# Kernel tuning notes

Measured on AMD Instinct MI355X. Metric: run time of the kernel, lower is better.

The kernel has to match this reference:

```python
import math
import jax, jax.numpy as jnp
import numpy as np

LMAX = 10
R_REF = 6371000.0
N = 1_000_000


def _sh_renorm(l, m, fourpi=True):
    base = math.sqrt((2.0 * l + 1.0) * math.factorial(l - abs(m)) / (4.0 * math.pi * math.factorial(l + abs(m))))
    if fourpi:
        base *= math.sqrt(4.0 * math.pi)
    return base


def _assoc_legendre(l, m, x):
    # P_l^m(x) via the standard stable recursion; l, m are Python ints (unrolled at trace time).
    pmm = jnp.ones_like(x)
    if m > 0:
        somx2 = jnp.sqrt(jnp.clip((1.0 - x) * (1.0 + x), 0.0, None))
        fact = 1.0
        for _ in range(1, m + 1):
            pmm = pmm * (-fact) * somx2
            fact += 2.0
    if l == m:
        return pmm
    pmmp1 = x * (2.0 * m + 1.0) * pmm
    if l == m + 1:
        return pmmp1
    pll = pmmp1
    for ll in range(m + 2, l + 1):
        pll = ((2.0 * ll - 1.0) * x * pmmp1 - (ll + m - 1.0) * pmm) / (ll - m)
        pmm = pmmp1
        pmmp1 = pll
    return pll


def _sh(m, l, phi, theta):
    cos_theta = jnp.clip(jnp.cos(theta), -1.0 + 1e-07, 1.0 - 1e-07)
    P_lm = _assoc_legendre(l, abs(m), cos_theta)
    K_lm = _sh_renorm(l, m)
    if m == 0:
        return K_lm * P_lm
    elif m > 0:
        return math.sqrt(2.0) * K_lm * jnp.cos(m * phi) * P_lm
    else:
        return math.sqrt(2.0) * K_lm * jnp.sin(-m * phi) * P_lm


def setup_inputs() -> dict:
    key = jax.random.key(0)
    k1, k2, k3 = jax.random.split(key, 3)
    lon = jax.random.uniform(k1, (N,), jnp.float32, -180.0, 180.0)
    lat = jax.random.uniform(k2, (N,), jnp.float32, -89.0, 89.0)
    r = R_REF * (1.0 + 0.01 * jax.random.uniform(k3, (N,), jnp.float32))
    return {"lonlatr": jnp.stack([lon, lat, r], axis=-1)}


def reference(lonlatr):
    lon, lat, r = lonlatr[:, 0], lonlatr[:, 1], lonlatr[:, 2]
    phi = jnp.deg2rad(lon + 180.0)
    theta = jnp.clip(jnp.deg2rad(90.0 - lat), 1e-07, math.pi - 1e-07)
    Y = []
    for l in range(LMAX + 1):
        for m in range(-l, l + 1):
            Y.append(_sh(m, l, phi, theta))
    Y = jnp.stack(Y, axis=-1)  # (N, (LMAX+1)^2)
    deg_idx = jnp.asarray(np.repeat(np.arange(LMAX + 1), 2 * np.arange(LMAX + 1) + 1), dtype=jnp.float32)
    radial_factor = (R_REF / r)[:, None] ** deg_idx[None, :]
    return Y * radial_factor
```

## Files before the change

### kernel.cpp

```cpp
#include <hip/hip_runtime.h>
#include <math.h>

#define LMAX 10
#define NCOL 121
#define PPB  64
#define TILE4 (PPB * NCOL / 4)

typedef float f4_t __attribute__((ext_vector_type(4)));

struct Tab {
    float K[66];
    float A[66];
    float B[66];
};

template<int M>
__device__ __forceinline__ void chain(const Tab& t, float* __restrict__ row,
                                      float pmm, float rfm, float rf, float x,
                                      float cm, float sm) {
    {
        float v = t.K[M * (M + 1) / 2 + M] * pmm * rfm;
        if constexpr (M == 0) row[0] = v;
        else { row[M * M + 2 * M] = v * cm; row[M * M] = v * sm; }
    }
    if constexpr (M < LMAX) {
        float p0 = pmm;
        float p1 = x * (float)(2 * M + 1) * pmm;
        float rfl = rfm * rf;
        {
            constexpr int L = M + 1;
            float v = t.K[L * (L + 1) / 2 + M] * p1 * rfl;
            if constexpr (M == 0) row[L * L + L] = v;
            else { row[L * L + L + M] = v * cm; row[L * L + L - M] = v * sm; }
        }
#pragma unroll
        for (int ll = M + 2; ll <= LMAX; ++ll) {
            int ti = ll * (ll + 1) / 2 + M;
            float p2 = t.A[ti] * x * p1 - t.B[ti] * p0;
            p0 = p1; p1 = p2;
            rfl *= rf;
            float v = t.K[ti] * p1 * rfl;
            int jb = ll * ll + ll;
            if constexpr (M == 0) row[jb] = v;
            else { row[jb + M] = v * cm; row[jb - M] = v * sm; }
        }
    }
}

template<bool FULL>
__global__ __launch_bounds__(256)
void sh_kernel(const float* __restrict__ in, float* __restrict__ out,
               int n, int blk_off, Tab t) {
    __shared__ f4_t lds4[TILE4];
    float* lds = (float*)lds4;

    const int bid = blockIdx.x + blk_off;
    const int p = threadIdx.x & 63;
    const int s = threadIdx.x >> 6;
    const long long gp = (long long)bid * PPB + p;

    if (FULL || gp < n) {
        const float lon = in[gp * 3 + 0];
        const float lat = in[gp * 3 + 1];
        const float r   = in[gp * 3 + 2];

        const float D2R  = 0.017453292519943295f;
        const float PI_F = 3.14159265358979323846f;

        float phi   = (lon + 180.0f) * D2R;
        float theta = fminf(fmaxf((90.0f - lat) * D2R, 1e-7f), PI_F - 1e-7f);
        float x = __cosf(theta);
        x = fminf(fmaxf(x, -1.0f + 1e-7f), 1.0f - 1e-7f);
        float somx2 = sqrtf(fmaxf((1.0f - x) * (1.0f + x), 0.0f));
        float rf  = 6371000.0f / r;
        float rf2 = rf * rf;
        float rf3 = rf2 * rf;
        float rf5 = rf3 * rf2;

        float c1, s1;
        __sincosf(phi, &s1, &c1);
        float c2 = c1 * c1 - s1 * s1, s2 = 2.0f * c1 * s1;
        float c3 = c2 * c1 - s2 * s1, s3 = s2 * c1 + c2 * s1;
        float c4 = c2 * c2 - s2 * s2, s4 = 2.0f * c2 * s2;
        float c5 = c4 * c1 - s4 * s1, s5 = s4 * c1 + c4 * s1;

        float sx2 = somx2 * somx2;
        float sx3 = sx2 * somx2;
        float sx5 = sx3 * sx2;

        float* row = lds + p * NCOL;

#define ROT(cm, sm, ck, sk) { float cn = cm * ck - sm * sk; sm = sm * ck + cm * sk; cm = cn; }

        switch (s) {
        case 0: {
            float pmm = 1.0f, rfm = 1.0f, cm = 1.0f, sm = 0.0f;
            chain<0>(t, row, pmm, rfm, rf, x, cm, sm);
            pmm *= -945.0f    * sx5; rfm *= rf5; ROT(cm, sm, c5, s5);
            chain<5>(t, row, pmm, rfm, rf, x, cm, sm);
            pmm *= -692835.0f * sx5; rfm *= rf5; ROT(cm, sm, c5, s5);
            chain<10>(t, row, pmm, rfm, rf, x, cm, sm);
        } break;
        case 1: {
            float pmm = -somx2, rfm = rf, cm = c1, sm = s1;
            chain<1>(t, row, pmm, rfm, rf, x, cm, sm);
            pmm *= -10395.0f * sx5; rfm *= rf5; ROT(cm, sm, c5, s5);
            chain<6>(t, row, pmm, rfm, rf, x, cm, sm);
            pmm *= -3315.0f  * sx3; rfm *= rf3; ROT(cm, sm, c3, s3);
            chain<9>(t, row, pmm, rfm, rf, x, cm, sm);
        } break;
        case 2: {
            float pmm = 3.0f * sx2, rfm = rf2, cm = c2, sm = s2;
            chain<2>(t, row, pmm, rfm, rf, x, cm, sm);
            pmm *= -45045.0f * sx5; rfm *= rf5; ROT(cm, sm, c5, s5);
            chain<7>(t, row, pmm, rfm, rf, x, cm, sm);
            pmm *= -15.0f * somx2;  rfm *= rf;  ROT(cm, sm, c1, s1);
            chain<8>(t, row, pmm, rfm, rf, x, cm, sm);
        } break;
        default: {
            float pmm = -15.0f * sx3, rfm = rf3, cm = c3, sm = s3;
            chain<3>(t, row, pmm, rfm, rf, x, cm, sm);
            pmm *= -7.0f * somx2; rfm *= rf; ROT(cm, sm, c1, s1);
            chain<4>(t, row, pmm, rfm, rf, x, cm, sm);
        } break;
        }
#undef ROT
    }
    __syncthreads();

    f4_t* __restrict__ dst = (f4_t*)out + (long long)bid * TILE4;
    if (FULL) {
#pragma unroll
        for (int k = 0; k < 7; ++k)
            dst[threadIdx.x + k * 256] = lds4[threadIdx.x + k * 256];
        if (threadIdx.x < TILE4 - 7 * 256)
            dst[threadIdx.x + 7 * 256] = lds4[threadIdx.x + 7 * 256];
    } else {
        const long long lim4 = ((long long)n * NCOL + 3) / 4;
        const long long base4 = (long long)bid * TILE4;
        for (int f = threadIdx.x; f < TILE4; f += 256) {
            if (base4 + f < lim4)
                dst[f] = lds4[f];
        }
    }
}

extern "C" void kernel_launch(void* const* d_in, const int* in_sizes, int n_in,
                              void* d_out, int out_size, void* d_ws, size_t ws_size,
                              hipStream_t stream) {
    const float* in = (const float*)d_in[0];
    float* out = (float*)d_out;
    const int n = in_sizes[0] / 3;

    Tab t;
    double fact[2 * LMAX + 1];
    fact[0] = 1.0;
    for (int i = 1; i <= 2 * LMAX; ++i) fact[i] = fact[i - 1] * (double)i;
    for (int l = 0; l <= LMAX; ++l) {
        for (int m = 0; m <= l; ++m) {
            int ti = l * (l + 1) / 2 + m;
            double k = sqrt((2.0 * l + 1.0) * fact[l - m] / fact[l + m]);
            if (m > 0) k *= sqrt(2.0);
            t.K[ti] = (float)k;
            if (l >= m + 2) {
                t.A[ti] = (float)((2.0 * l - 1.0) / (double)(l - m));
                t.B[ti] = (float)(((double)(l + m) - 1.0) / (double)(l - m));
            } else {
                t.A[ti] = 0.0f; t.B[ti] = 0.0f;
            }
        }
    }

    const int full_blocks = n / PPB;
    const int tail_pts    = n - full_blocks * PPB;
    if (full_blocks > 0)
        sh_kernel<true><<<full_blocks, 256, 0, stream>>>(in, out, n, 0, t);
    if (tail_pts > 0)
        sh_kernel<false><<<1, 256, 0, stream>>>(in, out, n, full_blocks, t);
}
```

Before: 103.0 us.

## Persistent double-buffered tiles with fp16 LDS staging and nontemporal stores

Replaces one-block-per-tile with a persistent grid of at most 1280 blocks that loop over tiles. Each block stores the previous tile from one LDS buffer while computing the next into the other. LDS staging moves to fp16 to halve shared memory and allow more resident blocks, and global writes use nontemporal stores. The fp16 round-trip loses precision in outputs stored as float, which risks failing accuracy tolerances.

```diff
diff --git a/kernel.cpp b/kernel.cpp
--- a/kernel.cpp
+++ b/kernel.cpp
@@ -1,9 +1,11 @@
 #include <hip/hip_runtime.h>
+#include <hip/hip_fp16.h>
 #include <math.h>
 
 #define LMAX 10
 #define NCOL 121
 #define PPB  64
+#define TILEH (PPB * NCOL)
 #define TILE4 (PPB * NCOL / 4)
 
 typedef float f4_t __attribute__((ext_vector_type(4)));
@@ -14,14 +16,14 @@
     float B[66];
 };
 
-template<int M>
-__device__ __forceinline__ void chain(const Tab& t, float* __restrict__ row,
+template<int M, typename ST, typename EMIT>
+__device__ __forceinline__ void chain(const Tab& t, ST* __restrict__ row,
                                       float pmm, float rfm, float rf, float x,
-                                      float cm, float sm) {
+                                      float cm, float sm, EMIT emit) {
     {
         float v = t.K[M * (M + 1) / 2 + M] * pmm * rfm;
-        if constexpr (M == 0) row[0] = v;
-        else { row[M * M + 2 * M] = v * cm; row[M * M] = v * sm; }
+        if constexpr (M == 0) emit(row, 0, v);
+        else { emit(row, M * M + 2 * M, v * cm); emit(row, M * M, v * sm); }
     }
     if constexpr (M < LMAX) {
         float p0 = pmm;
@@ -30,8 +32,8 @@
         {
             constexpr int L = M + 1;
             float v = t.K[L * (L + 1) / 2 + M] * p1 * rfl;
-            if constexpr (M == 0) row[L * L + L] = v;
-            else { row[L * L + L + M] = v * cm; row[L * L + L - M] = v * sm; }
+            if constexpr (M == 0) emit(row, L * L + L, v);
+            else { emit(row, L * L + L + M, v * cm); emit(row, L * L + L - M, v * sm); }
         }
 #pragma unroll
         for (int ll = M + 2; ll <= LMAX; ++ll) {
@@ -41,108 +43,156 @@
             rfl *= rf;
             float v = t.K[ti] * p1 * rfl;
             int jb = ll * ll + ll;
-            if constexpr (M == 0) row[jb] = v;
-            else { row[jb + M] = v * cm; row[jb - M] = v * sm; }
+            if constexpr (M == 0) emit(row, jb, v);
+            else { emit(row, jb + M, v * cm); emit(row, jb - M, v * sm); }
         }
     }
 }
 
-template<bool FULL>
-__global__ __launch_bounds__(256)
-void sh_kernel(const float* __restrict__ in, float* __restrict__ out,
-               int n, int blk_off, Tab t) {
-    __shared__ f4_t lds4[TILE4];
-    float* lds = (float*)lds4;
-
-    const int bid = blockIdx.x + blk_off;
+template<typename ST, typename EMIT>
+__device__ __forceinline__ void compute_tile(const float* __restrict__ in,
+                                             long long gp, int s, const Tab& t,
+                                             ST* __restrict__ row, EMIT emit) {
+    const float lon = in[gp * 3 + 0];
+    const float lat = in[gp * 3 + 1];
+    const float r   = in[gp * 3 + 2];
+
+    const float D2R  = 0.017453292519943295f;
+    const float PI_F = 3.14159265358979323846f;
+
+    float phi   = (lon + 180.0f) * D2R;
+    float theta = fminf(fmaxf((90.0f - lat) * D2R, 1e-7f), PI_F - 1e-7f);
+    float x = __cosf(theta);
+    x = fminf(fmaxf(x, -1.0f + 1e-7f), 1.0f - 1e-7f);
+    float somx2 = sqrtf(fmaxf((1.0f - x) * (1.0f + x), 0.0f));
+    float rf  = 6371000.0f / r;
+    float rf2 = rf * rf;
+    float rf3 = rf2 * rf;
+    float rf5 = rf3 * rf2;
+
+    float c1, s1;
+    __sincosf(phi, &s1, &c1);
+    float c2 = c1 * c1 - s1 * s1, s2 = 2.0f * c1 * s1;
+    float c3 = c2 * c1 - s2 * s1, s3 = s2 * c1 + c2 * s1;
+    float c5 = (c2 * c2 - s2 * s2) * c1 - 2.0f * c2 * s2 * s1;
+    float s5 = 2.0f * c2 * s2 * c1 + (c2 * c2 - s2 * s2) * s1;
+
+    float sx2 = somx2 * somx2;
+    float sx3 = sx2 * somx2;
+    float sx5 = sx3 * sx2;
+
+#define ROT(cm, sm, ck, sk) { float cn = cm * ck - sm * sk; sm = sm * ck + cm * sk; cm = cn; }
+    switch (s) {
+    case 0: {
+        float pmm = 1.0f, rfm = 1.0f, cm = 1.0f, sm = 0.0f;
+        chain<0>(t, row, pmm, rfm, rf, x, cm, sm, emit);
+        pmm *= -945.0f    * sx5; rfm *= rf5; ROT(cm, sm, c5, s5);
+        chain<5>(t, row, pmm, rfm, rf, x, cm, sm, emit);
+        pmm *= -692835.0f * sx5; rfm *= rf5; ROT(cm, sm, c5, s5);
+        chain<10>(t, row, pmm, rfm, rf, x, cm, sm, emit);
+    } break;
+    case 1: {
+        float pmm = -somx2, rfm = rf, cm = c1, sm = s1;
+        chain<1>(t, row, pmm, rfm, rf, x, cm, sm, emit);
+        pmm *= -10395.0f * sx5; rfm *= rf5; ROT(cm, sm, c5, s5);
+        chain<6>(t, row, pmm, rfm, rf, x, cm, sm, emit);
+        pmm *= -3315.0f  * sx3; rfm *= rf3; ROT(cm, sm, c3, s3);
+        chain<9>(t, row, pmm, rfm, rf, x, cm, sm, emit);
+    } break;
+    case 2: {
+        float pmm = 3.0f * sx2, rfm = rf2, cm = c2, sm = s2;
+        chain<2>(t, row, pmm, rfm, rf, x, cm, sm, emit);
+        pmm *= -45045.0f * sx5; rfm *= rf5; ROT(cm, sm, c5, s5);
+        chain<7>(t, row, pmm, rfm, rf, x, cm, sm, emit);
+        pmm *= -15.0f * somx2;  rfm *= rf;  ROT(cm, sm, c1, s1);
+        chain<8>(t, row, pmm, rfm, rf, x, cm, sm, emit);
+    } break;
+    default: {
+        float pmm = -15.0f * sx3, rfm = rf3, cm = c3, sm = s3;
+        chain<3>(t, row, pmm, rfm, rf, x, cm, sm, emit);
+        pmm *= -7.0f * somx2; rfm *= rf; ROT(cm, sm, c1, s1);
+        chain<4>(t, row, pmm, rfm, rf, x, cm, sm, emit);
+    } break;
+    }
+#undef ROT
+}
+
+struct EmitH {
+    __device__ void operator()(__half* row, int j, float v) const {
+        row[j] = __float2half(v);
+    }
+};
+struct EmitF {
+    __device__ void operator()(float* row, int j, float v) const {
+        row[j] = v;
+    }
+};
+
+__device__ __forceinline__ void store_tile(const __half* __restrict__ buf,
+                                           f4_t* __restrict__ dst) {
+    const uint2* __restrict__ src = (const uint2*)buf;
+#pragma unroll
+    for (int k = 0; k < 7; ++k) {
+        int i = threadIdx.x + k * 256;
+        uint2 h = src[i];
+        float2 fa = __half22float2(*(const __half2*)&h.x);
+        float2 fb = __half22float2(*(const __half2*)&h.y);
+        f4_t v = {fa.x, fa.y, fb.x, fb.y};
+        __builtin_nontemporal_store(v, &dst[i]);
+    }
+    if (threadIdx.x < TILE4 - 7 * 256) {
+        int i = threadIdx.x + 7 * 256;
+        uint2 h = src[i];
+        float2 fa = __half22float2(*(const __half2*)&h.x);
+        float2 fb = __half22float2(*(const __half2*)&h.y);
+        f4_t v = {fa.x, fa.y, fb.x, fb.y};
+        __builtin_nontemporal_store(v, &dst[i]);
+    }
+}
+
+__global__ __launch_bounds__(256, 5)
+void sh_main(const float* __restrict__ in, float* __restrict__ out,
+             int ntiles, Tab t) {
+    __shared__ __half lds[2][TILEH];
+
     const int p = threadIdx.x & 63;
     const int s = threadIdx.x >> 6;
-    const long long gp = (long long)bid * PPB + p;
-
-    if (FULL || gp < n) {
-        const float lon = in[gp * 3 + 0];
-        const float lat = in[gp * 3 + 1];
-        const float r   = in[gp * 3 + 2];
-
-        const float D2R  = 0.017453292519943295f;
-        const float PI_F = 3.14159265358979323846f;
-
-        float phi   = (lon + 180.0f) * D2R;
-        float theta = fminf(fmaxf((90.0f - lat) * D2R, 1e-7f), PI_F - 1e-7f);
-        float x = __cosf(theta);
-        x = fminf(fmaxf(x, -1.0f + 1e-7f), 1.0f - 1e-7f);
-        float somx2 = sqrtf(fmaxf((1.0f - x) * (1.0f + x), 0.0f));
-        float rf  = 6371000.0f / r;
-        float rf2 = rf * rf;
-        float rf3 = rf2 * rf;
-        float rf5 = rf3 * rf2;
-
-        float c1, s1;
-        __sincosf(phi, &s1, &c1);
-        float c2 = c1 * c1 - s1 * s1, s2 = 2.0f * c1 * s1;
-        float c3 = c2 * c1 - s2 * s1, s3 = s2 * c1 + c2 * s1;
-        float c4 = c2 * c2 - s2 * s2, s4 = 2.0f * c2 * s2;
-        float c5 = c4 * c1 - s4 * s1, s5 = s4 * c1 + c4 * s1;
-
-        float sx2 = somx2 * somx2;
-        float sx3 = sx2 * somx2;
-        float sx5 = sx3 * sx2;
-
-        float* row = lds + p * NCOL;
-
-#define ROT(cm, sm, ck, sk) { float cn = cm * ck - sm * sk; sm = sm * ck + cm * sk; cm = cn; }
-
-        switch (s) {
-        case 0: {
-            float pmm = 1.0f, rfm = 1.0f, cm = 1.0f, sm = 0.0f;
-            chain<0>(t, row, pmm, rfm, rf, x, cm, sm);
-            pmm *= -945.0f    * sx5; rfm *= rf5; ROT(cm, sm, c5, s5);
-            chain<5>(t, row, pmm, rfm, rf, x, cm, sm);
-            pmm *= -692835.0f * sx5; rfm *= rf5; ROT(cm, sm, c5, s5);
-            chain<10>(t, row, pmm, rfm, rf, x, cm, sm);
-        } break;
-        case 1: {
-            float pmm = -somx2, rfm = rf, cm = c1, sm = s1;
-            chain<1>(t, row, pmm, rfm, rf, x, cm, sm);
-            pmm *= -10395.0f * sx5; rfm *= rf5; ROT(cm, sm, c5, s5);
-            chain<6>(t, row, pmm, rfm, rf, x, cm, sm);
-            pmm *= -3315.0f  * sx3; rfm *= rf3; ROT(cm, sm, c3, s3);
-            chain<9>(t, row, pmm, rfm, rf, x, cm, sm);
-        } break;
-        case 2: {
-            float pmm = 3.0f * sx2, rfm = rf2, cm = c2, sm = s2;
-            chain<2>(t, row, pmm, rfm, rf, x, cm, sm);
-            pmm *= -45045.0f * sx5; rfm *= rf5; ROT(cm, sm, c5, s5);
-            chain<7>(t, row, pmm, rfm, rf, x, cm, sm);
-            pmm *= -15.0f * somx2;  rfm *= rf;  ROT(cm, sm, c1, s1);
-            chain<8>(t, row, pmm, rfm, rf, x, cm, sm);
-        } break;
-        default: {
-            float pmm = -15.0f * sx3, rfm = rf3, cm = c3, sm = s3;
-            chain<3>(t, row, pmm, rfm, rf, x, cm, sm);
-            pmm *= -7.0f * somx2; rfm *= rf; ROT(cm, sm, c1, s1);
-            chain<4>(t, row, pmm, rfm, rf, x, cm, sm);
-        } break;
-        }
-#undef ROT
-    }
+
+    int tile = blockIdx.x;
+    if (tile >= ntiles) return;
+
+    compute_tile(in, (long long)tile * PPB + p, s, t, &lds[0][p * NCOL], EmitH{});
     __syncthreads();
 
-    f4_t* __restrict__ dst = (f4_t*)out + (long long)bid * TILE4;
-    if (FULL) {
-#pragma unroll
-        for (int k = 0; k < 7; ++k)
-            dst[threadIdx.x + k * 256] = lds4[threadIdx.x + k * 256];
-        if (threadIdx.x < TILE4 - 7 * 256)
-            dst[threadIdx.x + 7 * 256] = lds4[threadIdx.x + 7 * 256];
-    } else {
-        const long long lim4 = ((long long)n * NCOL + 3) / 4;
-        const long long base4 = (long long)bid * TILE4;
-        for (int f = threadIdx.x; f < TILE4; f += 256) {
-            if (base4 + f < lim4)
-                dst[f] = lds4[f];
-        }
-    }
+    int buf = 0;
+    int prev = tile;
+    for (tile += gridDim.x; tile < ntiles; tile += gridDim.x) {
+        store_tile(lds[buf], (f4_t*)out + (long long)prev * TILE4);
+        compute_tile(in, (long long)tile * PPB + p, s, t, &lds[buf ^ 1][p * NCOL], EmitH{});
+        __syncthreads();
+        buf ^= 1;
+        prev = tile;
+    }
+    store_tile(lds[buf], (f4_t*)out + (long long)prev * TILE4);
+}
+
+__global__ __launch_bounds__(256)
+void sh_tail(const float* __restrict__ in, float* __restrict__ out,
+             int n, int tile0, Tab t) {
+    __shared__ float lds[PPB * NCOL];
+    const int p = threadIdx.x & 63;
+    const int s = threadIdx.x >> 6;
+    const long long gp = (long long)tile0 * PPB + p;
+    if (gp < n)
+        compute_tile(in, gp, s, t, &lds[p * NCOL], EmitF{});
+    __syncthreads();
+    const long long lim4 = ((long long)n * NCOL + 3) / 4;
+    const long long base4 = (long long)tile0 * TILE4;
+    f4_t* dst = (f4_t*)out + base4;
+    const f4_t* src = (const f4_t*)lds;
+    for (int f = threadIdx.x; f < TILE4; f += 256)
+        if (base4 + f < lim4)
+            __builtin_nontemporal_store(src[f], &dst[f]);
 }
 
 extern "C" void kernel_launch(void* const* d_in, const int* in_sizes, int n_in,
@@ -171,10 +221,11 @@
         }
     }
 
-    const int full_blocks = n / PPB;
-    const int tail_pts    = n - full_blocks * PPB;
-    if (full_blocks > 0)
-        sh_kernel<true><<<full_blocks, 256, 0, stream>>>(in, out, n, 0, t);
-    if (tail_pts > 0)
-        sh_kernel<false><<<1, 256, 0, stream>>>(in, out, n, full_blocks, t);
-}
+    const int full_tiles = n / PPB;
+    if (full_tiles > 0) {
+        int nblk = full_tiles < 1280 ? full_tiles : 1280;
+        sh_main<<<nblk, 256, 0, stream>>>(in, out, full_tiles, t);
+    }
+    if (n - full_tiles * PPB > 0)
+        sh_tail<<<1, 256, 0, stream>>>(in, out, n, full_tiles, t);
+}
```

After: 103.0 us. No clear change (+0.0%).
